# Optimization experiments

Hardware: AMD Instinct MI355X
Metric: run time of the kernel (lower is better)

## Reference

```python
import jax, jax.numpy as jnp
import numpy as np

TOP_K = 8
NUM_EXPERTS = 256
HIDDEN = 7168
NUM_TOKENS = 16384
NORM_TOPK_PROB = True


def setup_inputs() -> dict:
    key = jax.random.key(0)
    k1, k2 = jax.random.split(key)
    hidden_states = jax.random.normal(k1, (NUM_TOKENS, HIDDEN), dtype=jnp.float32)
    weight = jax.random.normal(k2, (NUM_EXPERTS, HIDDEN), dtype=jnp.float32) * 0.02
    return {"hidden_states": hidden_states, "weight": weight}


def reference(hidden_states, weight):
    # Router logits: [T, E] = [T, H] @ [E, H]^T
    logits = jnp.einsum("th,eh->te", hidden_states, weight)
    # Fused softmax + top-k (npu_moe_gating_top_k_softmax semantics):
    # softmax over experts, then take top-k probabilities and their indices.
    probs = jax.nn.softmax(logits, axis=-1)
    topk_weight, topk_idx = jax.lax.top_k(probs, TOP_K)  # [T, k]
    # row_idx: expert-major (column-major) flattened row indices, as the NPU op returns.
    T = logits.shape[0]
    row_idx = jnp.arange(T * TOP_K, dtype=jnp.int32).reshape(TOP_K, T).T  # [T, k]
    if TOP_K > 1 and NORM_TOPK_PROB:
        denominator = jnp.sum(topk_weight, axis=-1, keepdims=True) + 1e-20
        topk_weight = topk_weight / denominator
    topk_idx = topk_idx.astype(jnp.int32)
    return (topk_idx, topk_weight, row_idx)
```

## Files before the change

kernel.cpp:

```cpp
#include <hip/hip_runtime.h>
#include <hip/hip_bf16.h>

#define NTOK 16384
#define HID 7168
#define NEXP 256
#define TOPK 8

#define BT 64
#define BK 64
#define NCH (HID / BK)

typedef __bf16 bf16x8 __attribute__((ext_vector_type(8)));
typedef float  f32x16 __attribute__((ext_vector_type(16)));

__device__ __forceinline__ unsigned int f2bfb(float x) {
    unsigned int u = __float_as_uint(x);
    return (u + 0x7fffu + ((u >> 16) & 1u)) >> 16;
}

__global__ void wconv(const float* __restrict__ wt, unsigned short* __restrict__ wb) {
    const int i = blockIdx.x * 256 + threadIdx.x;
    const float4 v = ((const float4*)wt)[i];
    uint2 o;
    o.x = f2bfb(v.x) | (f2bfb(v.y) << 16);
    o.y = f2bfb(v.z) | (f2bfb(v.w) << 16);
    ((uint2*)wb)[i] = o;
}

__global__ void moe_rows(float* __restrict__ ob) {
    const int q = blockIdx.x * 256 + threadIdx.x;
    ob[262144 + q] = (float)((q & 7) * NTOK + (q >> 3));
}

template<bool PRECONV>
__global__ __launch_bounds__(512) void moe_gate_mfma(
    const float* __restrict__ hs,
    const float* __restrict__ wt,
    const unsigned short* __restrict__ wb,
    float* __restrict__ ob)
{
    __shared__ __align__(16) char smem[81920];

    const int tid  = threadIdx.x;
    const int t0   = blockIdx.x * BT;
    const int lane = tid & 63;
    const int wv   = tid >> 6;
    const int wm   = wv >> 2;
    const int wn   = wv & 3;

    const int arow = tid >> 4;
    const int acg  = tid & 15;
    const float* apt = hs + (size_t)(t0 + arow) * HID + acg * 4;
    const int aswz0 = (arow * 128 + acg * 8) ^ ((arow & 7) << 4);
    const int aswz1 = ((arow + 32) * 128 + acg * 8) ^ ((arow & 7) << 4);

    const int brow = tid >> 3;
    const int bkg  = tid & 7;
    const unsigned short* bpt = PRECONV ? (wb + (size_t)brow * HID + bkg * 8) : (const unsigned short*)0;
    const int bsw  = ((brow & 7) << 4);
    const int bofs0 = ((brow      ) * 128 + bkg * 16) ^ bsw;
    const int bofs1 = ((brow +  64) * 128 + bkg * 16) ^ bsw;
    const int bofs2 = ((brow + 128) * 128 + bkg * 16) ^ bsw;
    const int bofs3 = ((brow + 192) * 128 + bkg * 16) ^ bsw;

    const float* fpt = wt + (size_t)brow * HID + bkg * 8;

    const int kl   = (lane >> 5) * 16;
    const int swz  = (lane & 7) << 4;
    const int frA  = (wm * 32 + (lane & 31)) * 128;
    const int erB0 = (wn * 64 + (lane & 31)) * 128;
    const int erB1 = erB0 + 32 * 128;

    f32x16 acc0 = {};
    f32x16 acc1 = {};

    float4 ra0, ra1;
    uint4  rb0, rb1, rb2, rb3;
    float4 rf0, rf1, rf2, rf3, rf4, rf5, rf6, rf7;

    auto loadA = [&](int s) {
        ra0 = *(const float4*)(apt + s * BK);
        ra1 = *(const float4*)(apt + (size_t)32 * HID + s * BK);
    };
    auto loadB = [&](int s) {
        if constexpr (PRECONV) {
            rb0 = *(const uint4*)(bpt + s * BK);
            rb1 = *(const uint4*)(bpt + (size_t)64  * HID + s * BK);
            rb2 = *(const uint4*)(bpt + (size_t)128 * HID + s * BK);
            rb3 = *(const uint4*)(bpt + (size_t)192 * HID + s * BK);
        } else {
            const float* p = fpt + s * BK;
            rf0 = *(const float4*)(p);                         rf1 = *(const float4*)(p + 4);
            rf2 = *(const float4*)(p + (size_t)64 * HID);      rf3 = *(const float4*)(p + (size_t)64 * HID + 4);
            rf4 = *(const float4*)(p + (size_t)128 * HID);     rf5 = *(const float4*)(p + (size_t)128 * HID + 4);
            rf6 = *(const float4*)(p + (size_t)192 * HID);     rf7 = *(const float4*)(p + (size_t)192 * HID + 4);
        }
    };
    auto writeA = [&](char* bA) {
        uint2 u0, u1;
        u0.x = f2bfb(ra0.x) | (f2bfb(ra0.y) << 16);
        u0.y = f2bfb(ra0.z) | (f2bfb(ra0.w) << 16);
        u1.x = f2bfb(ra1.x) | (f2bfb(ra1.y) << 16);
        u1.y = f2bfb(ra1.z) | (f2bfb(ra1.w) << 16);
        *(uint2*)(bA + aswz0) = u0;
        *(uint2*)(bA + aswz1) = u1;
    };
    auto writeB = [&](char* bB) {
        if constexpr (PRECONV) {
            *(uint4*)(bB + bofs0) = rb0;
            *(uint4*)(bB + bofs1) = rb1;
            *(uint4*)(bB + bofs2) = rb2;
            *(uint4*)(bB + bofs3) = rb3;
        } else {
            uint4 u;
            u.x = f2bfb(rf0.x) | (f2bfb(rf0.y) << 16); u.y = f2bfb(rf0.z) | (f2bfb(rf0.w) << 16);
            u.z = f2bfb(rf1.x) | (f2bfb(rf1.y) << 16); u.w = f2bfb(rf1.z) | (f2bfb(rf1.w) << 16);
            *(uint4*)(bB + bofs0) = u;
            u.x = f2bfb(rf2.x) | (f2bfb(rf2.y) << 16); u.y = f2bfb(rf2.z) | (f2bfb(rf2.w) << 16);
            u.z = f2bfb(rf3.x) | (f2bfb(rf3.y) << 16); u.w = f2bfb(rf3.z) | (f2bfb(rf3.w) << 16);
            *(uint4*)(bB + bofs1) = u;
            u.x = f2bfb(rf4.x) | (f2bfb(rf4.y) << 16); u.y = f2bfb(rf4.z) | (f2bfb(rf4.w) << 16);
            u.z = f2bfb(rf5.x) | (f2bfb(rf5.y) << 16); u.w = f2bfb(rf5.z) | (f2bfb(rf5.w) << 16);
            *(uint4*)(bB + bofs2) = u;
            u.x = f2bfb(rf6.x) | (f2bfb(rf6.y) << 16); u.y = f2bfb(rf6.z) | (f2bfb(rf6.w) << 16);
            u.z = f2bfb(rf7.x) | (f2bfb(rf7.y) << 16); u.w = f2bfb(rf7.z) | (f2bfb(rf7.w) << 16);
            *(uint4*)(bB + bofs3) = u;
        }
    };
    auto compute = [&](const char* bA, const char* bB) {
        #pragma unroll
        for (int kk = 0; kk < 4; ++kk) {
            const int c = (kk * 32 + kl) ^ swz;
            bf16x8 a  = *(const bf16x8*)(bA + frA  + c);
            bf16x8 b0 = *(const bf16x8*)(bB + erB0 + c);
            bf16x8 b1 = *(const bf16x8*)(bB + erB1 + c);
            acc0 = __builtin_amdgcn_mfma_f32_32x32x16_bf16(a, b0, acc0, 0, 0, 0);
            acc1 = __builtin_amdgcn_mfma_f32_32x32x16_bf16(a, b1, acc1, 0, 0, 0);
        }
    };

    loadA(0); loadB(0);
    writeA(smem); writeB(smem + 16384);
    __syncthreads();
    for (int s = 0; s < NCH; ++s) {
        char* curA = smem + (s & 1) * 8192;
        char* curB = smem + 16384 + (s & 1) * 32768;
        if (s + 1 < NCH) { loadA(s + 1); loadB(s + 1); }
        compute(curA, curB);
        if (s + 1 < NCH) {
            writeA(smem + ((s + 1) & 1) * 8192);
            writeB(smem + 16384 + ((s + 1) & 1) * 32768);
        }
        __syncthreads();
    }

    float* ll = (float*)smem;
    {
        const int e0 = wn * 64 + (lane & 31);
        const int rb = wm * 32 + 4 * (lane >> 5);
        #pragma unroll
        for (int r = 0; r < 16; ++r) {
            const int tok = rb + (r & 3) + 8 * (r >> 2);
            ll[tok * 257 + e0]      = acc0[r];
            ll[tok * 257 + e0 + 32] = acc1[r];
        }
    }
    __syncthreads();

    if (tid < 64) {
        const float* lr = ll + tid * 257;
        float bv[TOPK]; int bi8[TOPK];
        #pragma unroll
        for (int k = 0; k < TOPK; ++k) { bv[k] = -1e30f; bi8[k] = 0; }
        for (int e = 0; e < NEXP; ++e) {
            const float v = lr[e];
            if (v > bv[TOPK - 1]) {
                int k = TOPK - 1;
                while (k > 0 && v > bv[k - 1]) {
                    bv[k] = bv[k - 1]; bi8[k] = bi8[k - 1]; --k;
                }
                bv[k] = v; bi8[k] = e;
            }
        }
        float ev[TOPK], ssum = 0.f;
        #pragma unroll
        for (int r = 0; r < TOPK; ++r) { ev[r] = expf(bv[r] - bv[0]); ssum += ev[r]; }
        const float inv = 1.0f / ssum;

        const int tg = t0 + tid;
        #pragma unroll
        for (int r = 0; r < TOPK; ++r) {
            ob[(size_t)tg * TOPK + r]          = (float)bi8[r];
            ob[131072 + (size_t)tg * TOPK + r] = ev[r] * inv;
        }
    }
}

extern "C" void kernel_launch(void* const* d_in, const int* in_sizes, int n_in,
                              void* d_out, int out_size, void* d_ws, size_t ws_size,
                              hipStream_t stream) {
    const float* hs = (const float*)d_in[0];
    const float* wt = (const float*)d_in[1];
    float* ob = (float*)d_out;

    if (ws_size >= (size_t)NEXP * HID * 2) {
        unsigned short* wb = (unsigned short*)d_ws;
        wconv<<<dim3(NEXP * HID / 4 / 256), dim3(256), 0, stream>>>(wt, wb);
        moe_gate_mfma<true><<<dim3(NTOK / BT), dim3(512), 0, stream>>>(hs, wt, wb, ob);
    } else {
        moe_gate_mfma<false><<<dim3(NTOK / BT), dim3(512), 0, stream>>>(hs, wt, nullptr, ob);
    }
    moe_rows<<<dim3(512), dim3(256), 0, stream>>>(ob);
}
```

Measured before the change: 255.0 us.

## Halve token tile to 32 and double-buffer global loads with two register sets

Halves the token tile per block to 32, giving 512 blocks instead of 256. Each of the 8 waves now computes a 32x32 expert slice with a single accumulator. Global-to-register loads are prefetched two stages ahead using two alternating register sets, and the LDS footprint drops so that more blocks can be resident per CU (launch bounds hint 4). The aim is more parallelism and better latency hiding on the memory-bound activation stream. The cost is that each weight tile is now re-read from L2 by twice as many blocks, and register pressure rises.

```diff
diff --git a/kernel.cpp b/kernel.cpp
--- a/kernel.cpp
+++ b/kernel.cpp
@@ -6,7 +6,7 @@
 #define NEXP 256
 #define TOPK 8
 
-#define BT 64
+#define BT 32
 #define BK 64
 #define NCH (HID / BK)
 
@@ -33,141 +33,149 @@
 }
 
 template<bool PRECONV>
-__global__ __launch_bounds__(512) void moe_gate_mfma(
+__global__ __launch_bounds__(512, 4) void moe_gate_mfma(
     const float* __restrict__ hs,
     const float* __restrict__ wt,
     const unsigned short* __restrict__ wb,
     float* __restrict__ ob)
 {
-    __shared__ __align__(16) char smem[81920];
+    __shared__ __align__(16) char smem[73728];
 
     const int tid  = threadIdx.x;
     const int t0   = blockIdx.x * BT;
     const int lane = tid & 63;
     const int wv   = tid >> 6;
-    const int wm   = wv >> 2;
-    const int wn   = wv & 3;
 
     const int arow = tid >> 4;
     const int acg  = tid & 15;
     const float* apt = hs + (size_t)(t0 + arow) * HID + acg * 4;
-    const int aswz0 = (arow * 128 + acg * 8) ^ ((arow & 7) << 4);
-    const int aswz1 = ((arow + 32) * 128 + acg * 8) ^ ((arow & 7) << 4);
+    const int aofs = (arow * 128 + acg * 8) ^ ((arow & 7) << 4);
 
     const int brow = tid >> 3;
     const int bkg  = tid & 7;
     const unsigned short* bpt = PRECONV ? (wb + (size_t)brow * HID + bkg * 8) : (const unsigned short*)0;
+    const float* fpt = wt + (size_t)brow * HID + bkg * 8;
     const int bsw  = ((brow & 7) << 4);
     const int bofs0 = ((brow      ) * 128 + bkg * 16) ^ bsw;
     const int bofs1 = ((brow +  64) * 128 + bkg * 16) ^ bsw;
     const int bofs2 = ((brow + 128) * 128 + bkg * 16) ^ bsw;
     const int bofs3 = ((brow + 192) * 128 + bkg * 16) ^ bsw;
 
-    const float* fpt = wt + (size_t)brow * HID + bkg * 8;
-
-    const int kl   = (lane >> 5) * 16;
-    const int swz  = (lane & 7) << 4;
-    const int frA  = (wm * 32 + (lane & 31)) * 128;
-    const int erB0 = (wn * 64 + (lane & 31)) * 128;
-    const int erB1 = erB0 + 32 * 128;
-
-    f32x16 acc0 = {};
-    f32x16 acc1 = {};
-
-    float4 ra0, ra1;
-    uint4  rb0, rb1, rb2, rb3;
-    float4 rf0, rf1, rf2, rf3, rf4, rf5, rf6, rf7;
-
-    auto loadA = [&](int s) {
-        ra0 = *(const float4*)(apt + s * BK);
-        ra1 = *(const float4*)(apt + (size_t)32 * HID + s * BK);
-    };
-    auto loadB = [&](int s) {
-        if constexpr (PRECONV) {
-            rb0 = *(const uint4*)(bpt + s * BK);
-            rb1 = *(const uint4*)(bpt + (size_t)64  * HID + s * BK);
-            rb2 = *(const uint4*)(bpt + (size_t)128 * HID + s * BK);
-            rb3 = *(const uint4*)(bpt + (size_t)192 * HID + s * BK);
-        } else {
-            const float* p = fpt + s * BK;
-            rf0 = *(const float4*)(p);                         rf1 = *(const float4*)(p + 4);
-            rf2 = *(const float4*)(p + (size_t)64 * HID);      rf3 = *(const float4*)(p + (size_t)64 * HID + 4);
-            rf4 = *(const float4*)(p + (size_t)128 * HID);     rf5 = *(const float4*)(p + (size_t)128 * HID + 4);
-            rf6 = *(const float4*)(p + (size_t)192 * HID);     rf7 = *(const float4*)(p + (size_t)192 * HID + 4);
-        }
-    };
-    auto writeA = [&](char* bA) {
-        uint2 u0, u1;
-        u0.x = f2bfb(ra0.x) | (f2bfb(ra0.y) << 16);
-        u0.y = f2bfb(ra0.z) | (f2bfb(ra0.w) << 16);
-        u1.x = f2bfb(ra1.x) | (f2bfb(ra1.y) << 16);
-        u1.y = f2bfb(ra1.z) | (f2bfb(ra1.w) << 16);
-        *(uint2*)(bA + aswz0) = u0;
-        *(uint2*)(bA + aswz1) = u1;
-    };
-    auto writeB = [&](char* bB) {
-        if constexpr (PRECONV) {
-            *(uint4*)(bB + bofs0) = rb0;
-            *(uint4*)(bB + bofs1) = rb1;
-            *(uint4*)(bB + bofs2) = rb2;
-            *(uint4*)(bB + bofs3) = rb3;
-        } else {
-            uint4 u;
-            u.x = f2bfb(rf0.x) | (f2bfb(rf0.y) << 16); u.y = f2bfb(rf0.z) | (f2bfb(rf0.w) << 16);
-            u.z = f2bfb(rf1.x) | (f2bfb(rf1.y) << 16); u.w = f2bfb(rf1.z) | (f2bfb(rf1.w) << 16);
-            *(uint4*)(bB + bofs0) = u;
-            u.x = f2bfb(rf2.x) | (f2bfb(rf2.y) << 16); u.y = f2bfb(rf2.z) | (f2bfb(rf2.w) << 16);
-            u.z = f2bfb(rf3.x) | (f2bfb(rf3.y) << 16); u.w = f2bfb(rf3.z) | (f2bfb(rf3.w) << 16);
-            *(uint4*)(bB + bofs1) = u;
-            u.x = f2bfb(rf4.x) | (f2bfb(rf4.y) << 16); u.y = f2bfb(rf4.z) | (f2bfb(rf4.w) << 16);
-            u.z = f2bfb(rf5.x) | (f2bfb(rf5.y) << 16); u.w = f2bfb(rf5.z) | (f2bfb(rf5.w) << 16);
-            *(uint4*)(bB + bofs2) = u;
-            u.x = f2bfb(rf6.x) | (f2bfb(rf6.y) << 16); u.y = f2bfb(rf6.z) | (f2bfb(rf6.w) << 16);
-            u.z = f2bfb(rf7.x) | (f2bfb(rf7.y) << 16); u.w = f2bfb(rf7.z) | (f2bfb(rf7.w) << 16);
-            *(uint4*)(bB + bofs3) = u;
-        }
-    };
+    const int kl  = (lane >> 5) * 16;
+    const int swz = (lane & 7) << 4;
+    const int frA = (lane & 31) * 128;
+    const int erB = (wv * 32 + (lane & 31)) * 128;
+
+    f32x16 acc = {};
+
+    float4 ra_0, ra_1;
+    uint4  rb0_0, rb1_0, rb2_0, rb3_0;
+    uint4  rb0_1, rb1_1, rb2_1, rb3_1;
+    float4 rf0_0, rf1_0, rf2_0, rf3_0, rf4_0, rf5_0, rf6_0, rf7_0;
+    float4 rf0_1, rf1_1, rf2_1, rf3_1, rf4_1, rf5_1, rf6_1, rf7_1;
+
+#define LOAD_SET(SET, s)                                                          \
+    do {                                                                          \
+        ra_##SET = *(const float4*)(apt + (s) * BK);                              \
+        if constexpr (PRECONV) {                                                  \
+            rb0_##SET = *(const uint4*)(bpt + (s) * BK);                          \
+            rb1_##SET = *(const uint4*)(bpt + (size_t)64  * HID + (s) * BK);      \
+            rb2_##SET = *(const uint4*)(bpt + (size_t)128 * HID + (s) * BK);      \
+            rb3_##SET = *(const uint4*)(bpt + (size_t)192 * HID + (s) * BK);      \
+        } else {                                                                  \
+            const float* p = fpt + (s) * BK;                                      \
+            rf0_##SET = *(const float4*)(p);                                      \
+            rf1_##SET = *(const float4*)(p + 4);                                  \
+            rf2_##SET = *(const float4*)(p + (size_t)64 * HID);                   \
+            rf3_##SET = *(const float4*)(p + (size_t)64 * HID + 4);               \
+            rf4_##SET = *(const float4*)(p + (size_t)128 * HID);                  \
+            rf5_##SET = *(const float4*)(p + (size_t)128 * HID + 4);              \
+            rf6_##SET = *(const float4*)(p + (size_t)192 * HID);                  \
+            rf7_##SET = *(const float4*)(p + (size_t)192 * HID + 4);              \
+        }                                                                         \
+    } while (0)
+
+#define WRITE_SET(SET, bA, bB)                                                    \
+    do {                                                                          \
+        uint2 ua;                                                                 \
+        ua.x = f2bfb(ra_##SET.x) | (f2bfb(ra_##SET.y) << 16);                     \
+        ua.y = f2bfb(ra_##SET.z) | (f2bfb(ra_##SET.w) << 16);                     \
+        *(uint2*)((bA) + aofs) = ua;                                              \
+        if constexpr (PRECONV) {                                                  \
+            *(uint4*)((bB) + bofs0) = rb0_##SET;                                  \
+            *(uint4*)((bB) + bofs1) = rb1_##SET;                                  \
+            *(uint4*)((bB) + bofs2) = rb2_##SET;                                  \
+            *(uint4*)((bB) + bofs3) = rb3_##SET;                                  \
+        } else {                                                                  \
+            uint4 u;                                                              \
+            u.x = f2bfb(rf0_##SET.x) | (f2bfb(rf0_##SET.y) << 16);                \
+            u.y = f2bfb(rf0_##SET.z) | (f2bfb(rf0_##SET.w) << 16);                \
+            u.z = f2bfb(rf1_##SET.x) | (f2bfb(rf1_##SET.y) << 16);                \
+            u.w = f2bfb(rf1_##SET.z) | (f2bfb(rf1_##SET.w) << 16);                \
+            *(uint4*)((bB) + bofs0) = u;                                          \
+            u.x = f2bfb(rf2_##SET.x) | (f2bfb(rf2_##SET.y) << 16);                \
+            u.y = f2bfb(rf2_##SET.z) | (f2bfb(rf2_##SET.w) << 16);                \
+            u.z = f2bfb(rf3_##SET.x) | (f2bfb(rf3_##SET.y) << 16);                \
+            u.w = f2bfb(rf3_##SET.z) | (f2bfb(rf3_##SET.w) << 16);                \
+            *(uint4*)((bB) + bofs1) = u;                                          \
+            u.x = f2bfb(rf4_##SET.x) | (f2bfb(rf4_##SET.y) << 16);                \
+            u.y = f2bfb(rf4_##SET.z) | (f2bfb(rf4_##SET.w) << 16);                \
+            u.z = f2bfb(rf5_##SET.x) | (f2bfb(rf5_##SET.y) << 16);                \
+            u.w = f2bfb(rf5_##SET.z) | (f2bfb(rf5_##SET.w) << 16);                \
+            *(uint4*)((bB) + bofs2) = u;                                          \
+            u.x = f2bfb(rf6_##SET.x) | (f2bfb(rf6_##SET.y) << 16);                \
+            u.y = f2bfb(rf6_##SET.z) | (f2bfb(rf6_##SET.w) << 16);                \
+            u.z = f2bfb(rf7_##SET.x) | (f2bfb(rf7_##SET.y) << 16);                \
+            u.w = f2bfb(rf7_##SET.z) | (f2bfb(rf7_##SET.w) << 16);                \
+            *(uint4*)((bB) + bofs3) = u;                                          \
+        }                                                                         \
+    } while (0)
+
+    char* const bA0 = smem;
+    char* const bA1 = smem + 4096;
+    char* const bB0 = smem + 8192;
+    char* const bB1 = smem + 40960;
+
     auto compute = [&](const char* bA, const char* bB) {
         #pragma unroll
         for (int kk = 0; kk < 4; ++kk) {
             const int c = (kk * 32 + kl) ^ swz;
-            bf16x8 a  = *(const bf16x8*)(bA + frA  + c);
-            bf16x8 b0 = *(const bf16x8*)(bB + erB0 + c);
-            bf16x8 b1 = *(const bf16x8*)(bB + erB1 + c);
-            acc0 = __builtin_amdgcn_mfma_f32_32x32x16_bf16(a, b0, acc0, 0, 0, 0);
-            acc1 = __builtin_amdgcn_mfma_f32_32x32x16_bf16(a, b1, acc1, 0, 0, 0);
+            bf16x8 a = *(const bf16x8*)(bA + frA + c);
+            bf16x8 b = *(const bf16x8*)(bB + erB + c);
+            acc = __builtin_amdgcn_mfma_f32_32x32x16_bf16(a, b, acc, 0, 0, 0);
         }
     };
 
-    loadA(0); loadB(0);
-    writeA(smem); writeB(smem + 16384);
+    LOAD_SET(0, 0);
+    LOAD_SET(1, 1);
+    WRITE_SET(0, bA0, bB0);
     __syncthreads();
-    for (int s = 0; s < NCH; ++s) {
-        char* curA = smem + (s & 1) * 8192;
-        char* curB = smem + 16384 + (s & 1) * 32768;
-        if (s + 1 < NCH) { loadA(s + 1); loadB(s + 1); }
-        compute(curA, curB);
-        if (s + 1 < NCH) {
-            writeA(smem + ((s + 1) & 1) * 8192);
-            writeB(smem + 16384 + ((s + 1) & 1) * 32768);
-        }
+
+    for (int s = 0; s < NCH; s += 2) {
+        if (s + 2 < NCH) LOAD_SET(0, s + 2);
+        compute(bA0, bB0);
+        WRITE_SET(1, bA1, bB1);
+        __syncthreads();
+
+        if (s + 3 < NCH) LOAD_SET(1, s + 3);
+        compute(bA1, bB1);
+        if (s + 2 < NCH) WRITE_SET(0, bA0, bB0);
         __syncthreads();
     }
 
     float* ll = (float*)smem;
     {
-        const int e0 = wn * 64 + (lane & 31);
-        const int rb = wm * 32 + 4 * (lane >> 5);
+        const int e0 = wv * 32 + (lane & 31);
+        const int rb = 4 * (lane >> 5);
         #pragma unroll
         for (int r = 0; r < 16; ++r) {
             const int tok = rb + (r & 3) + 8 * (r >> 2);
-            ll[tok * 257 + e0]      = acc0[r];
-            ll[tok * 257 + e0 + 32] = acc1[r];
+            ll[tok * 257 + e0] = acc[r];
         }
     }
     __syncthreads();
 
-    if (tid < 64) {
+    if (tid < BT) {
         const float* lr = ll + tid * 257;
         float bv[TOPK]; int bi8[TOPK];
         #pragma unroll
@@ -194,6 +202,8 @@
             ob[131072 + (size_t)tg * TOPK + r] = ev[r] * inv;
         }
     }
+#undef LOAD_SET
+#undef WRITE_SET
 }
 
 extern "C" void kernel_launch(void* const* d_in, const int* in_sizes, int n_in,
```

Result: no change. 254.3 us (-0.3%).

## Load weight fragments directly into registers and drop weight LDS staging

Applied to the files above, without the earlier changes.

Weight (B) operands are now loaded from global memory straight into MFMA register fragments for each wave, so the weight tile no longer passes through shared memory. Only the activation tile is staged in LDS. The loop is unrolled by two with register double-buffering, and each barrier waits only on LDS counters, not a full syncthreads. This removes LDS traffic and barrier cost for B, but each wave of a 4-way column group now reads its own weights from global/L2. Activation reads are duplicated across waves the same way, and register pressure goes up.

```diff
diff --git a/kernel.cpp b/kernel.cpp
--- a/kernel.cpp
+++ b/kernel.cpp
@@ -16,6 +16,17 @@
 __device__ __forceinline__ unsigned int f2bfb(float x) {
     unsigned int u = __float_as_uint(x);
     return (u + 0x7fffu + ((u >> 16) & 1u)) >> 16;
+}
+__device__ __forceinline__ bf16x8 asbf8(uint4 u) {
+    union { uint4 a; bf16x8 b; } c; c.a = u; return c.b;
+}
+__device__ __forceinline__ uint4 pk4(float4 p, float4 q) {
+    uint4 u;
+    u.x = f2bfb(p.x) | (f2bfb(p.y) << 16);
+    u.y = f2bfb(p.z) | (f2bfb(p.w) << 16);
+    u.z = f2bfb(q.x) | (f2bfb(q.y) << 16);
+    u.w = f2bfb(q.z) | (f2bfb(q.w) << 16);
+    return u;
 }
 
 __global__ void wconv(const float* __restrict__ wt, unsigned short* __restrict__ wb) {
@@ -33,13 +44,15 @@
 }
 
 template<bool PRECONV>
-__global__ __launch_bounds__(512) void moe_gate_mfma(
+__global__ __launch_bounds__(512) void moe_gate_v8(
     const float* __restrict__ hs,
     const float* __restrict__ wt,
     const unsigned short* __restrict__ wb,
     float* __restrict__ ob)
 {
-    __shared__ __align__(16) char smem[81920];
+    __shared__ __align__(16) char smem[66560];
+    char* const lbuf0 = smem;
+    char* const lbuf1 = smem + 8192;
 
     const int tid  = threadIdx.x;
     const int t0   = blockIdx.x * BT;
@@ -48,126 +61,124 @@
     const int wm   = wv >> 2;
     const int wn   = wv & 3;
 
-    const int arow = tid >> 4;
-    const int acg  = tid & 15;
-    const float* apt = hs + (size_t)(t0 + arow) * HID + acg * 4;
-    const int aswz0 = (arow * 128 + acg * 8) ^ ((arow & 7) << 4);
-    const int aswz1 = ((arow + 32) * 128 + acg * 8) ^ ((arow & 7) << 4);
-
-    const int brow = tid >> 3;
-    const int bkg  = tid & 7;
-    const unsigned short* bpt = PRECONV ? (wb + (size_t)brow * HID + bkg * 8) : (const unsigned short*)0;
-    const int bsw  = ((brow & 7) << 4);
-    const int bofs0 = ((brow      ) * 128 + bkg * 16) ^ bsw;
-    const int bofs1 = ((brow +  64) * 128 + bkg * 16) ^ bsw;
-    const int bofs2 = ((brow + 128) * 128 + bkg * 16) ^ bsw;
-    const int bofs3 = ((brow + 192) * 128 + bkg * 16) ^ bsw;
-
-    const float* fpt = wt + (size_t)brow * HID + bkg * 8;
-
-    const int kl   = (lane >> 5) * 16;
-    const int swz  = (lane & 7) << 4;
-    const int frA  = (wm * 32 + (lane & 31)) * 128;
-    const int erB0 = (wn * 64 + (lane & 31)) * 128;
-    const int erB1 = erB0 + 32 * 128;
+    const int tr = tid >> 3;
+    const int kg = tid & 7;
+    const float* apt = hs + (size_t)(t0 + tr) * HID + kg * 8;
+    const int aofs = (tr * 128 + kg * 16) ^ ((tr & 7) << 4);
+
+    const int kl  = (lane >> 5) * 16;
+    const int swz = (lane & 7) << 4;
+    const int frA = (wm * 32 + (lane & 31)) * 128;
+
+    const int e0 = wn * 64 + (lane & 31);
+    const unsigned short* bb0 = nullptr;
+    const float* fb0 = nullptr;
+    if constexpr (PRECONV) bb0 = wb + (size_t)e0 * HID + (lane >> 5) * 8;
+    else                   fb0 = wt + (size_t)e0 * HID + (lane >> 5) * 8;
 
     f32x16 acc0 = {};
     f32x16 acc1 = {};
 
-    float4 ra0, ra1;
-    uint4  rb0, rb1, rb2, rb3;
-    float4 rf0, rf1, rf2, rf3, rf4, rf5, rf6, rf7;
-
-    auto loadA = [&](int s) {
-        ra0 = *(const float4*)(apt + s * BK);
-        ra1 = *(const float4*)(apt + (size_t)32 * HID + s * BK);
-    };
-    auto loadB = [&](int s) {
-        if constexpr (PRECONV) {
-            rb0 = *(const uint4*)(bpt + s * BK);
-            rb1 = *(const uint4*)(bpt + (size_t)64  * HID + s * BK);
-            rb2 = *(const uint4*)(bpt + (size_t)128 * HID + s * BK);
-            rb3 = *(const uint4*)(bpt + (size_t)192 * HID + s * BK);
-        } else {
-            const float* p = fpt + s * BK;
-            rf0 = *(const float4*)(p);                         rf1 = *(const float4*)(p + 4);
-            rf2 = *(const float4*)(p + (size_t)64 * HID);      rf3 = *(const float4*)(p + (size_t)64 * HID + 4);
-            rf4 = *(const float4*)(p + (size_t)128 * HID);     rf5 = *(const float4*)(p + (size_t)128 * HID + 4);
-            rf6 = *(const float4*)(p + (size_t)192 * HID);     rf7 = *(const float4*)(p + (size_t)192 * HID + 4);
-        }
-    };
-    auto writeA = [&](char* bA) {
-        uint2 u0, u1;
-        u0.x = f2bfb(ra0.x) | (f2bfb(ra0.y) << 16);
-        u0.y = f2bfb(ra0.z) | (f2bfb(ra0.w) << 16);
-        u1.x = f2bfb(ra1.x) | (f2bfb(ra1.y) << 16);
-        u1.y = f2bfb(ra1.z) | (f2bfb(ra1.w) << 16);
-        *(uint2*)(bA + aswz0) = u0;
-        *(uint2*)(bA + aswz1) = u1;
-    };
-    auto writeB = [&](char* bB) {
-        if constexpr (PRECONV) {
-            *(uint4*)(bB + bofs0) = rb0;
-            *(uint4*)(bB + bofs1) = rb1;
-            *(uint4*)(bB + bofs2) = rb2;
-            *(uint4*)(bB + bofs3) = rb3;
-        } else {
-            uint4 u;
-            u.x = f2bfb(rf0.x) | (f2bfb(rf0.y) << 16); u.y = f2bfb(rf0.z) | (f2bfb(rf0.w) << 16);
-            u.z = f2bfb(rf1.x) | (f2bfb(rf1.y) << 16); u.w = f2bfb(rf1.z) | (f2bfb(rf1.w) << 16);
-            *(uint4*)(bB + bofs0) = u;
-            u.x = f2bfb(rf2.x) | (f2bfb(rf2.y) << 16); u.y = f2bfb(rf2.z) | (f2bfb(rf2.w) << 16);
-            u.z = f2bfb(rf3.x) | (f2bfb(rf3.y) << 16); u.w = f2bfb(rf3.z) | (f2bfb(rf3.w) << 16);
-            *(uint4*)(bB + bofs1) = u;
-            u.x = f2bfb(rf4.x) | (f2bfb(rf4.y) << 16); u.y = f2bfb(rf4.z) | (f2bfb(rf4.w) << 16);
-            u.z = f2bfb(rf5.x) | (f2bfb(rf5.y) << 16); u.w = f2bfb(rf5.z) | (f2bfb(rf5.w) << 16);
-            *(uint4*)(bB + bofs2) = u;
-            u.x = f2bfb(rf6.x) | (f2bfb(rf6.y) << 16); u.y = f2bfb(rf6.z) | (f2bfb(rf6.w) << 16);
-            u.z = f2bfb(rf7.x) | (f2bfb(rf7.y) << 16); u.w = f2bfb(rf7.z) | (f2bfb(rf7.w) << 16);
-            *(uint4*)(bB + bofs3) = u;
-        }
-    };
-    auto compute = [&](const char* bA, const char* bB) {
-        #pragma unroll
-        for (int kk = 0; kk < 4; ++kk) {
-            const int c = (kk * 32 + kl) ^ swz;
-            bf16x8 a  = *(const bf16x8*)(bA + frA  + c);
-            bf16x8 b0 = *(const bf16x8*)(bB + erB0 + c);
-            bf16x8 b1 = *(const bf16x8*)(bB + erB1 + c);
-            acc0 = __builtin_amdgcn_mfma_f32_32x32x16_bf16(a, b0, acc0, 0, 0, 0);
-            acc1 = __builtin_amdgcn_mfma_f32_32x32x16_bf16(a, b1, acc1, 0, 0, 0);
-        }
-    };
-
-    loadA(0); loadB(0);
-    writeA(smem); writeB(smem + 16384);
+    float4 fa00, fa01, fa10, fa11;
+    uint4 b00, b01, b02, b03, b04, b05, b06, b07;
+    uint4 b10, b11, b12, b13, b14, b15, b16, b17;
+
+#define LOADA(S, sidx)                                                        \
+    do {                                                                      \
+        fa##S##0 = *(const float4*)(apt + (size_t)(sidx) * BK);               \
+        fa##S##1 = *(const float4*)(apt + (size_t)(sidx) * BK + 4);           \
+    } while (0)
+
+#define LOADB(S, sidx)                                                        \
+    do {                                                                      \
+        if constexpr (PRECONV) {                                              \
+            const unsigned short* p0 = bb0 + (size_t)(sidx) * BK;             \
+            const unsigned short* p1 = p0 + (size_t)32 * HID;                 \
+            b##S##0 = *(const uint4*)(p0);                                    \
+            b##S##1 = *(const uint4*)(p0 + 16);                               \
+            b##S##2 = *(const uint4*)(p0 + 32);                               \
+            b##S##3 = *(const uint4*)(p0 + 48);                               \
+            b##S##4 = *(const uint4*)(p1);                                    \
+            b##S##5 = *(const uint4*)(p1 + 16);                               \
+            b##S##6 = *(const uint4*)(p1 + 32);                               \
+            b##S##7 = *(const uint4*)(p1 + 48);                               \
+        } else {                                                              \
+            const float* q0 = fb0 + (size_t)(sidx) * BK;                      \
+            const float* q1 = q0 + (size_t)32 * HID;                          \
+            b##S##0 = pk4(*(const float4*)(q0),      *(const float4*)(q0 + 4));  \
+            b##S##1 = pk4(*(const float4*)(q0 + 16), *(const float4*)(q0 + 20)); \
+            b##S##2 = pk4(*(const float4*)(q0 + 32), *(const float4*)(q0 + 36)); \
+            b##S##3 = pk4(*(const float4*)(q0 + 48), *(const float4*)(q0 + 52)); \
+            b##S##4 = pk4(*(const float4*)(q1),      *(const float4*)(q1 + 4));  \
+            b##S##5 = pk4(*(const float4*)(q1 + 16), *(const float4*)(q1 + 20)); \
+            b##S##6 = pk4(*(const float4*)(q1 + 32), *(const float4*)(q1 + 36)); \
+            b##S##7 = pk4(*(const float4*)(q1 + 48), *(const float4*)(q1 + 52)); \
+        }                                                                     \
+    } while (0)
+
+#define WRITEA(S, LB)                                                         \
+    do {                                                                      \
+        *(uint4*)((LB) + aofs) = pk4(fa##S##0, fa##S##1);                     \
+    } while (0)
+
+#define COMPUTE(S, LB)                                                        \
+    do {                                                                      \
+        bf16x8 a;                                                             \
+        a = *(const bf16x8*)((LB) + frA + ((0 * 32 + kl) ^ swz));             \
+        acc0 = __builtin_amdgcn_mfma_f32_32x32x16_bf16(a, asbf8(b##S##0), acc0, 0, 0, 0); \
+        acc1 = __builtin_amdgcn_mfma_f32_32x32x16_bf16(a, asbf8(b##S##4), acc1, 0, 0, 0); \
+        a = *(const bf16x8*)((LB) + frA + ((1 * 32 + kl) ^ swz));             \
+        acc0 = __builtin_amdgcn_mfma_f32_32x32x16_bf16(a, asbf8(b##S##1), acc0, 0, 0, 0); \
+        acc1 = __builtin_amdgcn_mfma_f32_32x32x16_bf16(a, asbf8(b##S##5), acc1, 0, 0, 0); \
+        a = *(const bf16x8*)((LB) + frA + ((2 * 32 + kl) ^ swz));             \
+        acc0 = __builtin_amdgcn_mfma_f32_32x32x16_bf16(a, asbf8(b##S##2), acc0, 0, 0, 0); \
+        acc1 = __builtin_amdgcn_mfma_f32_32x32x16_bf16(a, asbf8(b##S##6), acc1, 0, 0, 0); \
+        a = *(const bf16x8*)((LB) + frA + ((3 * 32 + kl) ^ swz));             \
+        acc0 = __builtin_amdgcn_mfma_f32_32x32x16_bf16(a, asbf8(b##S##3), acc0, 0, 0, 0); \
+        acc1 = __builtin_amdgcn_mfma_f32_32x32x16_bf16(a, asbf8(b##S##7), acc1, 0, 0, 0); \
+    } while (0)
+
+#define SOFTBAR()                                                             \
+    do {                                                                      \
+        asm volatile("s_waitcnt lgkmcnt(0)" ::: "memory");                    \
+        __builtin_amdgcn_s_barrier();                                         \
+    } while (0)
+
+    LOADA(0, 0); LOADA(1, 1); LOADB(0, 0);
+    WRITEA(0, lbuf0);
+    SOFTBAR();
+
+    for (int s = 0; s < NCH; s += 2) {
+        if (s + 2 < NCH) LOADA(0, s + 2);
+        LOADB(1, s + 1);
+        COMPUTE(0, lbuf0);
+        WRITEA(1, lbuf1);
+        SOFTBAR();
+
+        if (s + 3 < NCH) LOADA(1, s + 3);
+        if (s + 2 < NCH) LOADB(0, s + 2);
+        COMPUTE(1, lbuf1);
+        if (s + 2 < NCH) {
+            WRITEA(0, lbuf0);
+            SOFTBAR();
+        }
+    }
     __syncthreads();
-    for (int s = 0; s < NCH; ++s) {
-        char* curA = smem + (s & 1) * 8192;
-        char* curB = smem + 16384 + (s & 1) * 32768;
-        if (s + 1 < NCH) { loadA(s + 1); loadB(s + 1); }
-        compute(curA, curB);
-        if (s + 1 < NCH) {
-            writeA(smem + ((s + 1) & 1) * 8192);
-            writeB(smem + 16384 + ((s + 1) & 1) * 32768);
-        }
-        __syncthreads();
-    }
 
     float* ll = (float*)smem;
     {
-        const int e0 = wn * 64 + (lane & 31);
+        const int ec = wn * 64 + (lane & 31);
         const int rb = wm * 32 + 4 * (lane >> 5);
         #pragma unroll
         for (int r = 0; r < 16; ++r) {
             const int tok = rb + (r & 3) + 8 * (r >> 2);
-            ll[tok * 257 + e0]      = acc0[r];
-            ll[tok * 257 + e0 + 32] = acc1[r];
+            ll[tok * 257 + ec]      = acc0[r];
+            ll[tok * 257 + ec + 32] = acc1[r];
         }
     }
     __syncthreads();
 
-    if (tid < 64) {
+    if (tid < BT) {
         const float* lr = ll + tid * 257;
         float bv[TOPK]; int bi8[TOPK];
         #pragma unroll
@@ -194,6 +205,11 @@
             ob[131072 + (size_t)tg * TOPK + r] = ev[r] * inv;
         }
     }
+#undef LOADA
+#undef LOADB
+#undef WRITEA
+#undef COMPUTE
+#undef SOFTBAR
 }
 
 extern "C" void kernel_launch(void* const* d_in, const int* in_sizes, int n_in,
@@ -206,9 +222,9 @@
     if (ws_size >= (size_t)NEXP * HID * 2) {
         unsigned short* wb = (unsigned short*)d_ws;
         wconv<<<dim3(NEXP * HID / 4 / 256), dim3(256), 0, stream>>>(wt, wb);
-        moe_gate_mfma<true><<<dim3(NTOK / BT), dim3(512), 0, stream>>>(hs, wt, wb, ob);
+        moe_gate_v8<true><<<dim3(NTOK / BT), dim3(512), 0, stream>>>(hs, wt, wb, ob);
     } else {
-        moe_gate_mfma<false><<<dim3(NTOK / BT), dim3(512), 0, stream>>>(hs, wt, nullptr, ob);
+        moe_gate_v8<false><<<dim3(NTOK / BT), dim3(512), 0, stream>>>(hs, wt, nullptr, ob);
     }
     moe_rows<<<dim3(512), dim3(256), 0, stream>>>(ob);
 }
```

New measurement: 362.0 us. 41.9% more time.
